# Optimization experiments

Measured on AMD Instinct MI355X. Metric: run time of the kernel, lower is better.

Reference implementation:

```python
import jax, jax.numpy as jnp
import numpy as np

NEG = -1e30  # stand-in for -inf that keeps gradients finite


def setup_inputs() -> dict:
    key = jax.random.key(0)
    k0, k1, k2 = jax.random.split(key, 3)
    B, S, W, K = 48, 128, 4, 256
    logits = jax.random.normal(k0, (B, S, W, K), dtype=jnp.float32)
    T = jax.random.normal(k1, (B, K, K), dtype=jnp.float32)
    hamming_cost = jax.random.uniform(k2, (B, S, W, K), dtype=jnp.float32)
    tag_mask = jnp.ones((B, K, K), dtype=jnp.float32)
    text_mask = jnp.ones((B, S), dtype=jnp.int32)
    return dict(logits=logits, T=T, hamming_cost=hamming_cost,
                tag_mask=tag_mask, text_mask=text_mask)


def reference(logits, T, hamming_cost, tag_mask, text_mask):
    # Semi-Markov CRF partition function (use_transition_layer == 'True').
    B, S, W, K = logits.shape
    lg = jnp.transpose(logits, (1, 2, 0, 3))        # (S, W, B, K)
    hc = jnp.transpose(hamming_cost, (1, 2, 0, 3))  # (S, W, B, K)
    # emission score for a span of width w+1 ending at j, labeled k
    emit_all = (lg + hc) * tag_mask[:, 0, :]        # (S, W, B, K)
    tranT = T * tag_mask                            # (B, K, Kprev)
    w_idx = jnp.arange(W)

    # buf[w] = alpha[j - w]; rows with j - w < 0 held at NEG (excluded)
    buf0 = jnp.full((W, B, K), NEG, dtype=jnp.float32).at[0].set(0.0)

    def step(buf, inp):
        emit_j, j = inp  # emit_j: (W, B, K)
        # transition applies only when the previous alpha is a real segment
        # boundary (w < j); the w == j row connects to the initial state.
        tran = jnp.where((w_idx < j)[:, None, None, None], tranT[None], 0.0)
        # scores[w, b, k, kp] = alpha[j-w, b, kp] + T'[b, k, kp] + emit[w, b, k]
        scores = buf[:, :, None, :] + tran + emit_j[:, :, :, None]
        alpha_j = jax.nn.logsumexp(scores, axis=(0, 3))  # (B, K)
        buf = jnp.concatenate([alpha_j[None], buf[:-1]], axis=0)
        return buf, alpha_j

    _, alphas = jax.lax.scan(step, buf0, (emit_all, jnp.arange(S)))
    full = jnp.concatenate([jnp.zeros((1, B, K), dtype=jnp.float32), alphas], axis=0)
    ls = jax.nn.logsumexp(full, axis=-1)            # (S+1, B)
    lengths = jnp.sum(text_mask, axis=1)            # (B,)
    partition = ls[lengths, jnp.arange(B)]          # (B,)
    return partition[None]                          # (1, B) as in torch code
```

## Files before the change

### kernel.cpp

```cpp
#include <hip/hip_runtime.h>
#include <hip/hip_bf16.h>
#include <type_traits>

typedef __attribute__((ext_vector_type(8))) _Float16 half8;
typedef __attribute__((ext_vector_type(4))) _Float16 half4;
typedef __attribute__((ext_vector_type(2))) _Float16 half2;
typedef __attribute__((ext_vector_type(4))) float f32x4;

constexpr int CB = 48, CS = 128, CW = 4, CK = 256;
constexpr int LDP = 264;

__global__ void prep_eT_kernel(const f32x4* __restrict__ T,
                               const f32x4* __restrict__ tm,
                               half4* __restrict__ eT, int n4) {
    int i = blockIdx.x * 256 + threadIdx.x;
    if (i < n4) {
        f32x4 t = T[i], m = tm[i];
        half4 o;
        o[0] = (_Float16)__expf(t[0] * m[0]);
        o[1] = (_Float16)__expf(t[1] * m[1]);
        o[2] = (_Float16)__expf(t[2] * m[2]);
        o[3] = (_Float16)__expf(t[3] * m[3]);
        eT[i] = o;
    }
}

__global__ __launch_bounds__(256, 1)
void crf_scan_kernel(const float* __restrict__ logits,
                     const float* __restrict__ ham,
                     const _Float16* __restrict__ eT,
                     const float* __restrict__ tag_mask,
                     const int* __restrict__ text_mask,
                     float* __restrict__ out) {
    const int b = blockIdx.x;
    const int tid = (int)threadIdx.x;
    const int wv = tid >> 6;
    const int lane = tid & 63;
    const int l16 = lane & 15;
    const int g4 = lane >> 4;

    __shared__ alignas(16) _Float16 ebuf[4 * LDP];
    __shared__ float red[4];
    __shared__ int len_s;

    if (tid == 0) len_s = 0;
    __syncthreads();
    if (tid < CS) atomicAdd(&len_s, text_mask[b * CS + tid]);
    ebuf[3 * LDP + tid] = (_Float16)1.0f;

    const float tm0 = tag_mask[(size_t)b * CK * CK + tid];

    half8 bfr[8][4];
    const _Float16* eTb = eT + (size_t)b * CK * CK;
#pragma unroll
    for (int c = 0; c < 8; ++c)
#pragma unroll
        for (int t = 0; t < 4; ++t) {
            int k = wv * 64 + t * 16 + l16;
            bfr[c][t] = *(const half8*)(eTb + (size_t)k * CK + c * 32 + g4 * 8);
        }

    const float* lgb = logits + (size_t)b * CS * CW * CK;
    const float* hcb = ham    + (size_t)b * CS * CW * CK;

    half8 af[8];
    {
        const _Float16 iv = ((l16 & 3) == 3) ? (_Float16)1.0f : (_Float16)0.0f;
        half8 v;
#pragma unroll
        for (int i = 0; i < 8; ++i) v[i] = iv;
#pragma unroll
        for (int c = 0; c < 8; ++c) af[c] = v;
    }

    float mr[4] = {0.0f, 0.0f, 0.0f, 0.0f};
    float ls_prev = __logf(256.0f) - 2.0f;
    float out_r = __logf(256.0f);
    float e_last = 0.0f, M_last = 0.0f;

    float lgp[4][4], hcp[4][4];
#pragma unroll
    for (int s = 0; s < 4; ++s)
#pragma unroll
        for (int w = 0; w < 4; ++w) {
            int idx = s * (CW * CK) + w * CK + tid;
            lgp[s][w] = lgb[idx];
            hcp[s][w] = hcb[idx];
        }

    __syncthreads();
    const int len = len_s;

    const half2 one2 = {(_Float16)1.0f, (_Float16)1.0f};

    auto step = [&](int j, auto uc, auto firstc) {
        constexpr int u = uc.value;
        constexpr bool first = firstc.value;
        constexpr int sp = (u + 3) & 3;

        if ((l16 & 3) == sp) {
#pragma unroll
            for (int c = 0; c < 8; ++c)
                af[c] = *(const half8*)(ebuf + sp * LDP + c * 32 + g4 * 8);
        }

        float em_w[4];
#pragma unroll
        for (int w = 0; w < 4; ++w)
            em_w[w] = (lgp[u][w] + hcp[u][w]) * tm0;

        {
            int jn = (j + 4 < CS) ? j + 4 : 0;
#pragma unroll
            for (int w = 0; w < 4; ++w) {
                int idx = jn * (CW * CK) + w * CK + tid;
                lgp[u][w] = lgb[idx];
                hcp[u][w] = hcb[idx];
            }
        }

        const float C = mr[sp];
        float E[4];
#pragma unroll
        for (int r = 0; r < 4; ++r)
            E[r] = __expf(mr[r] + em_w[(u + 3 - r) & 3] - C);

        float rs0 = 0.0f, rs1 = 0.0f;
#pragma unroll
        for (int c = 0; c < 8; ++c) {
#pragma unroll
            for (int p = 0; p < 4; p += 2) {
                half2 h0 = {af[c][2 * p], af[c][2 * p + 1]};
                half2 h1 = {af[c][2 * p + 2], af[c][2 * p + 3]};
                rs0 = __builtin_amdgcn_fdot2(h0, one2, rs0, false);
                rs1 = __builtin_amdgcn_fdot2(h1, one2, rs1, false);
            }
        }
        float rs = rs0 + rs1;
        rs += __shfl_xor(rs, 16, 64);
        rs += __shfl_xor(rs, 32, 64);
        float sum_prev = __shfl(rs, sp, 64);

        float lsj = C + __logf(sum_prev);
        if (j == len) out_r = lsj;
        float delta = lsj - ls_prev;
        ls_prev = lsj;
        float Mj = lsj + delta;
        float scl = __expf(C - Mj);

        f32x4 acc[4];
#pragma unroll
        for (int t = 0; t < 4; ++t) acc[t] = (f32x4){0.0f, 0.0f, 0.0f, 0.0f};
#pragma unroll
        for (int c = 0; c < 8; ++c)
#pragma unroll
            for (int t = 0; t < 4; ++t)
                acc[t] = __builtin_amdgcn_mfma_f32_16x16x32_f16(af[c], bfr[c][t], acc[t], 0, 0, 0);

        float S = 0.0f;
#pragma unroll
        for (int r = 0; r < 4; ++r) {
            float v01 = (g4 & 1) ? acc[1][r] : acc[0][r];
            float v23 = (g4 & 1) ? acc[3][r] : acc[2][r];
            float yv  = (g4 & 2) ? v23 : v01;
            if (first) {
                const int w = (u + 3 - r) & 3;
                if (w == j) yv = 256.0f;
                else if (w > j) yv = 0.0f;
            }
            S = fmaf(yv, E[r], S);
        }
        float e = S * scl;
        ebuf[u * LDP + tid] = (_Float16)e;
        e_last = e;
        M_last = Mj;
        mr[u] = Mj;

        asm volatile("s_waitcnt lgkmcnt(0)" ::: "memory");
        __builtin_amdgcn_s_barrier();
        __builtin_amdgcn_sched_barrier(0);
    };

#define IC(v) std::integral_constant<int, v>{}
#define BC(v) std::integral_constant<bool, v>{}
    step(0, IC(0), BC(true));
    step(1, IC(1), BC(true));
    step(2, IC(2), BC(true));
    step(3, IC(3), BC(true));
    for (int jj = 4; jj < CS; jj += 4) {
        step(jj + 0, IC(0), BC(false));
        step(jj + 1, IC(1), BC(false));
        step(jj + 2, IC(2), BC(false));
        step(jj + 3, IC(3), BC(false));
    }
#undef IC
#undef BC

    float s = e_last;
#pragma unroll
    for (int o = 32; o; o >>= 1) s += __shfl_xor(s, o, 64);
    if (lane == 0) red[wv] = s;
    __syncthreads();
    if (tid == 0) {
        float tot = red[0] + red[1] + red[2] + red[3];
        float ls_full = M_last + __logf(tot);
        if (len == CS) out_r = ls_full;
        out[b] = out_r;
    }
}

extern "C" void kernel_launch(void* const* d_in, const int* in_sizes, int n_in,
                              void* d_out, int out_size, void* d_ws, size_t ws_size,
                              hipStream_t stream) {
    const float* logits    = (const float*)d_in[0];
    const float* T         = (const float*)d_in[1];
    const float* ham       = (const float*)d_in[2];
    const float* tag_mask  = (const float*)d_in[3];
    const int*   text_mask = (const int*)d_in[4];
    float* out = (float*)d_out;

    _Float16* eT = (_Float16*)d_ws;
    int n4 = CB * CK * CK / 4;
    prep_eT_kernel<<<(n4 + 255) / 256, 256, 0, stream>>>(
        (const f32x4*)T, (const f32x4*)tag_mask, (half4*)eT, n4);
    crf_scan_kernel<<<CB, 256, 0, stream>>>(logits, ham, eT, tag_mask, text_mask, out);
}
```

Before: 193.5 us.

## Split scan over 8 waves, compute row sums via MFMA, predict scale a step ahead

Each batch block now runs 512 threads (8 waves), and each wave owns 32 output labels instead of 64, which halves the per-wave MFMA chain on the serial recurrence critical path. The previous-alpha row sum is now computed with an MFMA against a ones vector instead of fdot2 plus shuffles. The max/scale estimate for the next step is extrapolated one step further ahead, so the exp scale is off the current step's dependency chain. The cost is extra MFMAs for the sum, a deeper emission prefetch split across two labels per thread, and four of every sixteen lanes doing the stores. The looser extrapolation also carries some risk of fp16 overflow or underflow.

```diff
diff --git a/kernel.cpp b/kernel.cpp
--- a/kernel.cpp
+++ b/kernel.cpp
@@ -4,7 +4,6 @@
 
 typedef __attribute__((ext_vector_type(8))) _Float16 half8;
 typedef __attribute__((ext_vector_type(4))) _Float16 half4;
-typedef __attribute__((ext_vector_type(2))) _Float16 half2;
 typedef __attribute__((ext_vector_type(4))) float f32x4;
 
 constexpr int CB = 48, CS = 128, CW = 4, CK = 256;
@@ -25,7 +24,7 @@
     }
 }
 
-__global__ __launch_bounds__(256, 1)
+__global__ __launch_bounds__(512, 2)
 void crf_scan_kernel(const float* __restrict__ logits,
                      const float* __restrict__ ham,
                      const _Float16* __restrict__ eT,
@@ -38,27 +37,29 @@
     const int lane = tid & 63;
     const int l16 = lane & 15;
     const int g4 = lane >> 4;
+    const int kb = wv * 32;
+    const int k0 = kb + l16;
+    const int k1 = kb + 16 + l16;
 
     __shared__ alignas(16) _Float16 ebuf[4 * LDP];
-    __shared__ float red[4];
+    __shared__ float red[8];
     __shared__ int len_s;
 
     if (tid == 0) len_s = 0;
     __syncthreads();
     if (tid < CS) atomicAdd(&len_s, text_mask[b * CS + tid]);
-    ebuf[3 * LDP + tid] = (_Float16)1.0f;
-
-    const float tm0 = tag_mask[(size_t)b * CK * CK + tid];
-
-    half8 bfr[8][4];
+    if (tid < CK) ebuf[3 * LDP + tid] = (_Float16)1.0f;
+
+    const float tm0a = tag_mask[(size_t)b * CK * CK + k0];
+    const float tm0b = tag_mask[(size_t)b * CK * CK + k1];
+
+    half8 bfr[8][2];
     const _Float16* eTb = eT + (size_t)b * CK * CK;
 #pragma unroll
-    for (int c = 0; c < 8; ++c)
-#pragma unroll
-        for (int t = 0; t < 4; ++t) {
-            int k = wv * 64 + t * 16 + l16;
-            bfr[c][t] = *(const half8*)(eTb + (size_t)k * CK + c * 32 + g4 * 8);
-        }
+    for (int c = 0; c < 8; ++c) {
+        bfr[c][0] = *(const half8*)(eTb + (size_t)k0 * CK + c * 32 + g4 * 8);
+        bfr[c][1] = *(const half8*)(eTb + (size_t)k1 * CK + c * 32 + g4 * 8);
+    }
 
     const float* lgb = logits + (size_t)b * CS * CW * CK;
     const float* hcb = ham    + (size_t)b * CS * CW * CK;
@@ -76,27 +77,34 @@
     float mr[4] = {0.0f, 0.0f, 0.0f, 0.0f};
     float ls_prev = __logf(256.0f) - 2.0f;
     float out_r = __logf(256.0f);
-    float e_last = 0.0f, M_last = 0.0f;
-
-    float lgp[4][4], hcp[4][4];
-#pragma unroll
-    for (int s = 0; s < 4; ++s)
+    float e_last0 = 0.0f, e_last1 = 0.0f, M_last = 0.0f;
+    float Mcur = __logf(256.0f) + 2.0f;
+    float scl  = __expf(0.0f - Mcur);
+
+    float lgp[2][4][2], hcp[2][4][2];
+#pragma unroll
+    for (int d = 0; d < 2; ++d)
 #pragma unroll
         for (int w = 0; w < 4; ++w) {
-            int idx = s * (CW * CK) + w * CK + tid;
-            lgp[s][w] = lgb[idx];
-            hcp[s][w] = hcb[idx];
+            int i0 = d * (CW * CK) + w * CK;
+            lgp[d][w][0] = lgb[i0 + k0];
+            lgp[d][w][1] = lgb[i0 + k1];
+            hcp[d][w][0] = hcb[i0 + k0];
+            hcp[d][w][1] = hcb[i0 + k1];
         }
 
     __syncthreads();
     const int len = len_s;
 
-    const half2 one2 = {(_Float16)1.0f, (_Float16)1.0f};
+    half8 ones;
+#pragma unroll
+    for (int i = 0; i < 8; ++i) ones[i] = (_Float16)1.0f;
 
     auto step = [&](int j, auto uc, auto firstc) {
         constexpr int u = uc.value;
         constexpr bool first = firstc.value;
         constexpr int sp = (u + 3) & 3;
+        constexpr int p = u & 1;
 
         if ((l16 & 3) == sp) {
 #pragma unroll
@@ -104,77 +112,78 @@
                 af[c] = *(const half8*)(ebuf + sp * LDP + c * 32 + g4 * 8);
         }
 
-        float em_w[4];
-#pragma unroll
-        for (int w = 0; w < 4; ++w)
-            em_w[w] = (lgp[u][w] + hcp[u][w]) * tm0;
+        float em[4][2];
+#pragma unroll
+        for (int w = 0; w < 4; ++w) {
+            em[w][0] = (lgp[p][w][0] + hcp[p][w][0]) * tm0a;
+            em[w][1] = (lgp[p][w][1] + hcp[p][w][1]) * tm0b;
+        }
 
         {
-            int jn = (j + 4 < CS) ? j + 4 : 0;
+            int jn = (j + 2 < CS) ? j + 2 : 0;
+            int i0 = jn * (CW * CK);
 #pragma unroll
             for (int w = 0; w < 4; ++w) {
-                int idx = jn * (CW * CK) + w * CK + tid;
-                lgp[u][w] = lgb[idx];
-                hcp[u][w] = hcb[idx];
+                lgp[p][w][0] = lgb[i0 + w * CK + k0];
+                lgp[p][w][1] = lgb[i0 + w * CK + k1];
+                hcp[p][w][0] = hcb[i0 + w * CK + k0];
+                hcp[p][w][1] = hcb[i0 + w * CK + k1];
             }
         }
 
         const float C = mr[sp];
-        float E[4];
-#pragma unroll
-        for (int r = 0; r < 4; ++r)
-            E[r] = __expf(mr[r] + em_w[(u + 3 - r) & 3] - C);
-
-        float rs0 = 0.0f, rs1 = 0.0f;
-#pragma unroll
-        for (int c = 0; c < 8; ++c) {
-#pragma unroll
-            for (int p = 0; p < 4; p += 2) {
-                half2 h0 = {af[c][2 * p], af[c][2 * p + 1]};
-                half2 h1 = {af[c][2 * p + 2], af[c][2 * p + 3]};
-                rs0 = __builtin_amdgcn_fdot2(h0, one2, rs0, false);
-                rs1 = __builtin_amdgcn_fdot2(h1, one2, rs1, false);
+        float E0[4], E1[4];
+#pragma unroll
+        for (int r = 0; r < 4; ++r) {
+            const int w = (u + 3 - r) & 3;
+            E0[r] = __expf(mr[r] + em[w][0] - C);
+            E1[r] = __expf(mr[r] + em[w][1] - C);
+        }
+        mr[u] = Mcur;
+
+        f32x4 a0 = {0,0,0,0}, a1 = {0,0,0,0};
+        f32x4 b0 = {0,0,0,0}, b1 = {0,0,0,0};
+        f32x4 s0 = {0,0,0,0}, s1 = {0,0,0,0};
+#pragma unroll
+        for (int c = 0; c < 4; ++c) {
+            a0 = __builtin_amdgcn_mfma_f32_16x16x32_f16(af[c], bfr[c][0], a0, 0, 0, 0);
+            b0 = __builtin_amdgcn_mfma_f32_16x16x32_f16(af[c], bfr[c][1], b0, 0, 0, 0);
+            s0 = __builtin_amdgcn_mfma_f32_16x16x32_f16(af[c], ones, s0, 0, 0, 0);
+        }
+#pragma unroll
+        for (int c = 4; c < 8; ++c) {
+            a1 = __builtin_amdgcn_mfma_f32_16x16x32_f16(af[c], bfr[c][0], a1, 0, 0, 0);
+            b1 = __builtin_amdgcn_mfma_f32_16x16x32_f16(af[c], bfr[c][1], b1, 0, 0, 0);
+            s1 = __builtin_amdgcn_mfma_f32_16x16x32_f16(af[c], ones, s1, 0, 0, 0);
+        }
+        f32x4 y0 = a0 + a1, y1 = b0 + b1, rsum = s0 + s1;
+
+        float S0 = 0.0f, S1 = 0.0f;
+#pragma unroll
+        for (int r = 0; r < 4; ++r) {
+            float v0 = y0[r], v1 = y1[r];
+            if (first) {
+                const int w = (u + 3 - r) & 3;
+                if (w == j) { v0 = 256.0f; v1 = 256.0f; }
+                else if (w > j) { v0 = 0.0f; v1 = 0.0f; }
             }
-        }
-        float rs = rs0 + rs1;
-        rs += __shfl_xor(rs, 16, 64);
-        rs += __shfl_xor(rs, 32, 64);
-        float sum_prev = __shfl(rs, sp, 64);
-
-        float lsj = C + __logf(sum_prev);
+            S0 = fmaf(v0, E0[r], S0);
+            S1 = fmaf(v1, E1[r], S1);
+        }
+        float e0 = S0 * scl, e1 = S1 * scl;
+        if (g4 == 0) {
+            ebuf[u * LDP + k0] = (_Float16)e0;
+            ebuf[u * LDP + k1] = (_Float16)e1;
+        }
+        e_last0 = e0; e_last1 = e1; M_last = Mcur;
+
+        float lsj = C + __logf(rsum[sp]);
         if (j == len) out_r = lsj;
         float delta = lsj - ls_prev;
         ls_prev = lsj;
-        float Mj = lsj + delta;
-        float scl = __expf(C - Mj);
-
-        f32x4 acc[4];
-#pragma unroll
-        for (int t = 0; t < 4; ++t) acc[t] = (f32x4){0.0f, 0.0f, 0.0f, 0.0f};
-#pragma unroll
-        for (int c = 0; c < 8; ++c)
-#pragma unroll
-            for (int t = 0; t < 4; ++t)
-                acc[t] = __builtin_amdgcn_mfma_f32_16x16x32_f16(af[c], bfr[c][t], acc[t], 0, 0, 0);
-
-        float S = 0.0f;
-#pragma unroll
-        for (int r = 0; r < 4; ++r) {
-            float v01 = (g4 & 1) ? acc[1][r] : acc[0][r];
-            float v23 = (g4 & 1) ? acc[3][r] : acc[2][r];
-            float yv  = (g4 & 2) ? v23 : v01;
-            if (first) {
-                const int w = (u + 3 - r) & 3;
-                if (w == j) yv = 256.0f;
-                else if (w > j) yv = 0.0f;
-            }
-            S = fmaf(yv, E[r], S);
-        }
-        float e = S * scl;
-        ebuf[u * LDP + tid] = (_Float16)e;
-        e_last = e;
-        M_last = Mj;
-        mr[u] = Mj;
+        float Mn = lsj + 2.0f * delta;
+        scl = __expf(Mcur - Mn);
+        Mcur = Mn;
 
         asm volatile("s_waitcnt lgkmcnt(0)" ::: "memory");
         __builtin_amdgcn_s_barrier();
@@ -196,13 +205,15 @@
 #undef IC
 #undef BC
 
-    float s = e_last;
+    float s = (g4 == 0) ? (e_last0 + e_last1) : 0.0f;
 #pragma unroll
     for (int o = 32; o; o >>= 1) s += __shfl_xor(s, o, 64);
     if (lane == 0) red[wv] = s;
     __syncthreads();
     if (tid == 0) {
-        float tot = red[0] + red[1] + red[2] + red[3];
+        float tot = 0.0f;
+#pragma unroll
+        for (int i = 0; i < 8; ++i) tot += red[i];
         float ls_full = M_last + __logf(tot);
         if (len == CS) out_r = ls_full;
         out[b] = out_r;
@@ -223,5 +234,5 @@
     int n4 = CB * CK * CK / 4;
     prep_eT_kernel<<<(n4 + 255) / 256, 256, 0, stream>>>(
         (const f32x4*)T, (const f32x4*)tag_mask, (half4*)eT, n4);
-    crf_scan_kernel<<<CB, 256, 0, stream>>>(logits, ham, eT, tag_mask, text_mask, out);
+    crf_scan_kernel<<<CB, 512, 0, stream>>>(logits, ham, eT, tag_mask, text_mask, out);
 }
```

Result: slower. 209.4 us (+8.2%).

## Compute row sums via MFMA and defer scale estimate off critical path

Applied to the files above, without the earlier changes.

Replaces the fdot2 row-sum reduction and its cross-lane shuffles with extra MFMA instructions against a ones vector, interleaved with the main transition MFMAs. The normalization scale for step j is now predicted from the previous step's log-sum (extrapolated by twice the delta), so the log/exp chain no longer sits between the A-fragment load and the MFMA issue. This shortens the serial dependency per step, at the cost of extra MFMA work and a less accurate stabilizer that could raise fp16 overflow/underflow risk.

```diff
diff --git a/kernel.cpp b/kernel.cpp
--- a/kernel.cpp
+++ b/kernel.cpp
@@ -4,7 +4,6 @@
 
 typedef __attribute__((ext_vector_type(8))) _Float16 half8;
 typedef __attribute__((ext_vector_type(4))) _Float16 half4;
-typedef __attribute__((ext_vector_type(2))) _Float16 half2;
 typedef __attribute__((ext_vector_type(4))) float f32x4;
 
 constexpr int CB = 48, CS = 128, CW = 4, CK = 256;
@@ -77,6 +76,8 @@
     float ls_prev = __logf(256.0f) - 2.0f;
     float out_r = __logf(256.0f);
     float e_last = 0.0f, M_last = 0.0f;
+    float Mcur = __logf(256.0f) + 2.0f;
+    float scl  = __expf(0.0f - Mcur);
 
     float lgp[4][4], hcp[4][4];
 #pragma unroll
@@ -91,7 +92,9 @@
     __syncthreads();
     const int len = len_s;
 
-    const half2 one2 = {(_Float16)1.0f, (_Float16)1.0f};
+    half8 ones;
+#pragma unroll
+    for (int i = 0; i < 8; ++i) ones[i] = (_Float16)1.0f;
 
     auto step = [&](int j, auto uc, auto firstc) {
         constexpr int u = uc.value;
@@ -124,38 +127,21 @@
 #pragma unroll
         for (int r = 0; r < 4; ++r)
             E[r] = __expf(mr[r] + em_w[(u + 3 - r) & 3] - C);
-
-        float rs0 = 0.0f, rs1 = 0.0f;
+        mr[u] = Mcur;
+
+        f32x4 acc[4];
+#pragma unroll
+        for (int t = 0; t < 4; ++t) acc[t] = (f32x4){0.0f, 0.0f, 0.0f, 0.0f};
+        f32x4 s0 = {0, 0, 0, 0}, s1 = {0, 0, 0, 0};
 #pragma unroll
         for (int c = 0; c < 8; ++c) {
-#pragma unroll
-            for (int p = 0; p < 4; p += 2) {
-                half2 h0 = {af[c][2 * p], af[c][2 * p + 1]};
-                half2 h1 = {af[c][2 * p + 2], af[c][2 * p + 3]};
-                rs0 = __builtin_amdgcn_fdot2(h0, one2, rs0, false);
-                rs1 = __builtin_amdgcn_fdot2(h1, one2, rs1, false);
-            }
-        }
-        float rs = rs0 + rs1;
-        rs += __shfl_xor(rs, 16, 64);
-        rs += __shfl_xor(rs, 32, 64);
-        float sum_prev = __shfl(rs, sp, 64);
-
-        float lsj = C + __logf(sum_prev);
-        if (j == len) out_r = lsj;
-        float delta = lsj - ls_prev;
-        ls_prev = lsj;
-        float Mj = lsj + delta;
-        float scl = __expf(C - Mj);
-
-        f32x4 acc[4];
-#pragma unroll
-        for (int t = 0; t < 4; ++t) acc[t] = (f32x4){0.0f, 0.0f, 0.0f, 0.0f};
-#pragma unroll
-        for (int c = 0; c < 8; ++c)
 #pragma unroll
             for (int t = 0; t < 4; ++t)
                 acc[t] = __builtin_amdgcn_mfma_f32_16x16x32_f16(af[c], bfr[c][t], acc[t], 0, 0, 0);
+            if (c & 1) s1 = __builtin_amdgcn_mfma_f32_16x16x32_f16(af[c], ones, s1, 0, 0, 0);
+            else       s0 = __builtin_amdgcn_mfma_f32_16x16x32_f16(af[c], ones, s0, 0, 0, 0);
+        }
+        f32x4 rsum = s0 + s1;
 
         float S = 0.0f;
 #pragma unroll
@@ -173,8 +159,15 @@
         float e = S * scl;
         ebuf[u * LDP + tid] = (_Float16)e;
         e_last = e;
-        M_last = Mj;
-        mr[u] = Mj;
+        M_last = Mcur;
+
+        float lsj = C + __logf(rsum[sp]);
+        if (j == len) out_r = lsj;
+        float delta = lsj - ls_prev;
+        ls_prev = lsj;
+        float Mn = lsj + 2.0f * delta;
+        scl = __expf(Mcur - Mn);
+        Mcur = Mn;
 
         asm volatile("s_waitcnt lgkmcnt(0)" ::: "memory");
         __builtin_amdgcn_s_barrier();
```

Measured after the change: 176.7 us (median of 2 runs). 8.7% less time.
